# Kernel optimization log

Measured on AMD Instinct MI355X. Metric: run time of the kernel, lower is better.

The kernel has to match this reference:

```python
import jax, jax.numpy as jnp
import numpy as np

MAXHD = 100.0
MAXV = 40.0
LSTM_UNITS = 20
IN_DIM = 12


def setup_inputs() -> dict:
    key = jax.random.key(0)
    ks = jax.random.split(key, 10)
    nveh, nt = 8192, 512
    leadfol_inputs = jax.random.normal(ks[0], (nveh, nt, IN_DIM), dtype=jnp.float32)
    true_traj = jax.random.normal(ks[1], (nveh, nt), dtype=jnp.float32)
    hidden_states = jnp.zeros((2, nveh, LSTM_UNITS), dtype=jnp.float32)
    s = 0.1
    # LSTM kernel/recurrent kernel/bias (keras gate order: i, f, c, o)
    W_k = jax.random.normal(ks[2], (IN_DIM, 4 * LSTM_UNITS), dtype=jnp.float32) * s
    W_r = jax.random.normal(ks[3], (LSTM_UNITS, 4 * LSTM_UNITS), dtype=jnp.float32) * s
    b_l = jnp.zeros((4 * LSTM_UNITS,), dtype=jnp.float32)
    # dense (10, relu) and lc_actions (3)
    W_d = jax.random.normal(ks[4], (LSTM_UNITS, 10), dtype=jnp.float32) * s
    b_d = jnp.zeros((10,), dtype=jnp.float32)
    W_lc = jax.random.normal(ks[5], (10, 3), dtype=jnp.float32) * s
    b_lc = jnp.zeros((3,), dtype=jnp.float32)
    return {"leadfol_inputs": leadfol_inputs, "true_traj": true_traj,
            "hidden_states": hidden_states, "W_k": W_k, "W_r": W_r, "b_l": b_l,
            "W_d": W_d, "b_d": b_d, "W_lc": W_lc, "b_lc": b_lc}


def reference(leadfol_inputs, true_traj, hidden_states, W_k, W_r, b_l, W_d, b_d, W_lc, b_lc):
    # time-major for scan: (nt, nveh, ...)
    lf_t = jnp.swapaxes(leadfol_inputs, 0, 1)
    pos_t = jnp.swapaxes(true_traj, 0, 1)

    def step(carry, xt):
        h, c = carry
        pos, lf = xt  # pos: (nveh,), lf: (nveh, 12)
        lead_hd = (lf[:, :3] - pos[:, None]) / MAXHD
        fol_hd = (pos[:, None] - lf[:, 3:6]) / MAXHD
        spds = lf[:, 6:] / MAXV
        x = jnp.concatenate([lead_hd, fol_hd, spds], axis=1)
        x = jnp.where(jnp.isnan(x), jnp.ones_like(x), x)
        z = x @ W_k + h @ W_r + b_l
        zi, zf, zg, zo = jnp.split(z, 4, axis=1)
        c = jax.nn.sigmoid(zf) * c + jax.nn.sigmoid(zi) * jnp.tanh(zg)
        h = jax.nn.sigmoid(zo) * jnp.tanh(c)
        d = jax.nn.relu(h @ W_d + b_d)
        lc = d @ W_lc + b_lc
        return (h, c), lc

    (h, c), lc_t = jax.lax.scan(step, (hidden_states[0], hidden_states[1]), (pos_t, lf_t))
    pred_lc_action = jnp.swapaxes(lc_t, 0, 1)  # (nveh, nt, 3)
    return (true_traj, pred_lc_action, h, c)
```

## Files before the change

### kernel.cpp

```cpp
#include <hip/hip_runtime.h>

#define NVEH 8192
#define NT   512

typedef short bf16x8 __attribute__((ext_vector_type(8)));
typedef float f32x4  __attribute__((ext_vector_type(4)));

__device__ __forceinline__ float fsig(float x) {
    float e = __builtin_amdgcn_exp2f(-1.44269504f * x);
    return __builtin_amdgcn_rcpf(1.0f + e);
}
__device__ __forceinline__ float ftanh(float x) {
    float e = __builtin_amdgcn_exp2f(-2.88539008f * x);
    return 2.0f * __builtin_amdgcn_rcpf(1.0f + e) - 1.0f;
}
__device__ __forceinline__ unsigned short f2bf(float f) {
    union { float f; unsigned u; } vv; vv.f = f;
    unsigned r = vv.u + 0x7fff + ((vv.u >> 16) & 1);
    return (unsigned short)(r >> 16);
}

__device__ __forceinline__ void lds_barrier() {
    asm volatile("s_waitcnt lgkmcnt(0)" ::: "memory");
    __builtin_amdgcn_s_barrier();
    asm volatile("" ::: "memory");
}

__global__ __launch_bounds__(256) void lstm_scan_kernel(
    const float* __restrict__ lead, const float* __restrict__ traj,
    const float* __restrict__ hidden,
    const float* __restrict__ W_k, const float* __restrict__ W_r,
    const float* __restrict__ b_l, const float* __restrict__ W_d,
    const float* __restrict__ b_d, const float* __restrict__ W_lc,
    const float* __restrict__ b_lc,
    float* __restrict__ out_lc, float* __restrict__ out_h, float* __restrict__ out_c)
{
    __shared__ alignas(16) unsigned short row[2][16][40];

    const int tid  = threadIdx.x;
    const int wid  = tid >> 6;
    const int lane = tid & 63;
    const int q    = lane >> 4;
    const int v    = lane & 15;
    const int gv   = blockIdx.x * 16 + v;

    const int ntile = (wid < 2) ? 2 : (wid == 2) ? 1 : 0;

    bf16x8 aW[2]; f32x4 cB[2];
    float h32[2], cst[2];
    int uu[2];
    #pragma unroll
    for (int l = 0; l < 2; ++l) {
        if (l < ntile) {
            const int tt = 2 * wid + l;
            #pragma unroll
            for (int j = 0; j < 8; ++j) {
                int k  = q * 8 + j;
                int qv = v >> 2, rv = v & 3;
                int u  = (tt < 4) ? (8 * (tt >> 1) + 2 * qv + (tt & 1)) : (16 + qv);
                int col = rv * 20 + u;
                float w = (k < 12) ? W_k[k * 80 + col] : W_r[(k - 12) * 80 + col];
                aW[l][j] = (short)f2bf(w);
            }
            uu[l] = (tt < 4) ? (8 * (tt >> 1) + 2 * q + (tt & 1)) : (16 + q);
            #pragma unroll
            for (int reg = 0; reg < 4; ++reg)
                cB[l][reg] = b_l[reg * 20 + uu[l]];
            h32[l] = hidden[(size_t)gv * 20 + uu[l]];
            cst[l] = hidden[(size_t)NVEH * 20 + (size_t)gv * 20 + uu[l]];
        }
    }

    if (wid < 2) {
        unsigned pk = (unsigned)f2bf(h32[0]) | ((unsigned)f2bf(h32[1]) << 16);
        *(unsigned*)&row[0][v][12 + 8 * wid + 2 * q] = pk;
    } else if (wid == 2) {
        row[0][v][28 + q] = f2bf(h32[0]);
    }

    const float* lf = lead + (size_t)gv * NT * 12;
    const float* ps = traj + (size_t)gv * NT;
    float* lcout    = out_lc + (size_t)gv * NT * 3;

    bf16x8 aH = {}; f32x4 cD = {};
    float wlc[4][3] = {}; float pb0[3] = {};
    float Ac[4], Bc[4];
    float4 rA = make_float4(0.f,0.f,0.f,0.f), rB = rA, rC = rA;
    float pA = 0.f, pB = 0.f, pC = 0.f;
    if (wid == 3) {
        #pragma unroll
        for (int j = 0; j < 8; ++j) {
            int k = q * 8 + j;
            aH[j] = (v < 10 && k >= 12) ? (short)f2bf(W_d[(k - 12) * 10 + v]) : (short)0;
        }
        #pragma unroll
        for (int reg = 0; reg < 4; ++reg) {
            int m = 4 * q + reg;
            cD[reg] = (m < 10) ? b_d[m] : 0.0f;
            #pragma unroll
            for (int j = 0; j < 3; ++j)
                wlc[reg][j] = (m < 10) ? W_lc[m * 3 + j] : 0.0f;
        }
        #pragma unroll
        for (int j = 0; j < 3; ++j) pb0[j] = (q == 0) ? b_lc[j] : 0.0f;

        #pragma unroll
        for (int i = 0; i < 4; ++i) {
            int e = 4 * q + i;
            if (e < 3)      { Ac[i] =  0.01f;  Bc[i] = -0.01f; }
            else if (e < 6) { Ac[i] = -0.01f;  Bc[i] =  0.01f; }
            else            { Ac[i] =  0.025f; Bc[i] =  0.0f;  }
        }

        #pragma unroll
        for (int s = 0; s < 2; ++s) {
            float4 r0 = make_float4(0.f,0.f,0.f,0.f); float p0s = 0.f;
            if (q < 3) r0 = *(const float4*)(lf + 12 * s + q * 4);
            if (q < 2) p0s = ps[s];
            if (q < 3) {
                float xv[4] = { r0.x, r0.y, r0.z, r0.w };
                #pragma unroll
                for (int i = 0; i < 4; ++i) {
                    float x = fmaf(xv[i], Ac[i], p0s * Bc[i]);
                    xv[i] = (x == x) ? x : 1.0f;
                }
                unsigned pk0 = (unsigned)f2bf(xv[0]) | ((unsigned)f2bf(xv[1]) << 16);
                unsigned pk1 = (unsigned)f2bf(xv[2]) | ((unsigned)f2bf(xv[3]) << 16);
                *(uint2*)&row[s][v][4 * q] = make_uint2(pk0, pk1);
            }
        }
        if (q < 3) {
            rA = *(const float4*)(lf + 12 * 2 + q * 4);
            rB = *(const float4*)(lf + 12 * 3 + q * 4);
            rC = *(const float4*)(lf + 12 * 4 + q * 4);
        }
        if (q < 2) { pA = ps[2]; pB = ps[3]; pC = ps[4]; }
    }

    lds_barrier();
    bf16x8 bx = *(const bf16x8*)&row[0][v][8 * q];

    for (int t = 0; t < NT; ++t) {
        const int nxt = (t + 1) & 1;

        if (wid < 3) {
            f32x4 z0 = __builtin_amdgcn_mfma_f32_16x16x32_bf16(aW[0], bx, cB[0], 0, 0, 0);
            f32x4 z1;
            if (ntile == 2)
                z1 = __builtin_amdgcn_mfma_f32_16x16x32_bf16(aW[1], bx, cB[1], 0, 0, 0);

            {
                float si = fsig(z0[0]);
                float sf = fsig(z0[1]);
                float tg = ftanh(z0[2]);
                float so = fsig(z0[3]);
                float cn = fmaf(sf, cst[0], si * tg);
                cst[0] = cn;
                h32[0] = so * ftanh(cn);
            }
            if (ntile == 2) {
                float si = fsig(z1[0]);
                float sf = fsig(z1[1]);
                float tg = ftanh(z1[2]);
                float so = fsig(z1[3]);
                float cn = fmaf(sf, cst[1], si * tg);
                cst[1] = cn;
                h32[1] = so * ftanh(cn);
            }

            if (wid < 2) {
                unsigned pk = (unsigned)f2bf(h32[0]) | ((unsigned)f2bf(h32[1]) << 16);
                *(unsigned*)&row[nxt][v][12 + 8 * wid + 2 * q] = pk;
            } else {
                row[nxt][v][28 + q] = f2bf(h32[0]);
            }
        }

        lds_barrier();
        bf16x8 bxn = *(const bf16x8*)&row[nxt][v][8 * q];

        if (wid == 3) {
            f32x4 d = __builtin_amdgcn_mfma_f32_16x16x32_bf16(aH, bxn, cD, 0, 0, 0);
            float dr[4];
            #pragma unroll
            for (int reg = 0; reg < 4; ++reg) dr[reg] = fmaxf(d[reg], 0.0f);
            float p[3];
            #pragma unroll
            for (int j = 0; j < 3; ++j) {
                float acc = pb0[j];
                #pragma unroll
                for (int reg = 0; reg < 4; ++reg) acc = fmaf(dr[reg], wlc[reg][j], acc);
                acc += __shfl_xor(acc, 16);
                acc += __shfl_xor(acc, 32);
                p[j] = acc;
            }
            if (q == (t & 3)) {
                float* o = lcout + (size_t)t * 3;
                *(float2*)o = make_float2(p[0], p[1]);
                o[2] = p[2];
            }

            if (q < 3) {
                float xv[4] = { rA.x, rA.y, rA.z, rA.w };
                #pragma unroll
                for (int i = 0; i < 4; ++i) {
                    float x = fmaf(xv[i], Ac[i], pA * Bc[i]);
                    xv[i] = (x == x) ? x : 1.0f;
                }
                unsigned pk0 = (unsigned)f2bf(xv[0]) | ((unsigned)f2bf(xv[1]) << 16);
                unsigned pk1 = (unsigned)f2bf(xv[2]) | ((unsigned)f2bf(xv[3]) << 16);
                *(uint2*)&row[t & 1][v][4 * q] = make_uint2(pk0, pk1);
            }
            rA = rB; rB = rC; pA = pB; pB = pC;
            int tn = (t + 5 < NT) ? (t + 5) : (NT - 1);
            if (q < 3) rC = *(const float4*)(lf + 12 * tn + q * 4);
            if (q < 2) pC = ps[tn];
        }

        bx = bxn;
    }

    if (wid < 3) {
        #pragma unroll
        for (int l = 0; l < 2; ++l) {
            if (l < ntile) {
                out_h[(size_t)gv * 20 + uu[l]] = h32[l];
                out_c[(size_t)gv * 20 + uu[l]] = cst[l];
            }
        }
    }
}

extern "C" void kernel_launch(void* const* d_in, const int* in_sizes, int n_in,
                              void* d_out, int out_size, void* d_ws, size_t ws_size,
                              hipStream_t stream) {
    const float* lead   = (const float*)d_in[0];
    const float* traj   = (const float*)d_in[1];
    const float* hidden = (const float*)d_in[2];
    const float* W_k    = (const float*)d_in[3];
    const float* W_r    = (const float*)d_in[4];
    const float* b_l    = (const float*)d_in[5];
    const float* W_d    = (const float*)d_in[6];
    const float* b_d    = (const float*)d_in[7];
    const float* W_lc   = (const float*)d_in[8];
    const float* b_lc   = (const float*)d_in[9];

    float* out    = (float*)d_out;
    float* out_tt = out;
    float* out_lc = out + (size_t)NVEH * NT;
    float* out_h  = out_lc + (size_t)NVEH * NT * 3;
    float* out_c  = out_h + (size_t)NVEH * 20;

    hipMemcpyAsync(out_tt, traj, (size_t)NVEH * NT * sizeof(float),
                   hipMemcpyDeviceToDevice, stream);

    lstm_scan_kernel<<<dim3(NVEH / 16), dim3(256), 0, stream>>>(
        lead, traj, hidden, W_k, W_r, b_l, W_d, b_d, W_lc, b_lc,
        out_lc, out_h, out_c);
}
```

Before: 657.6 us.

## Process two 16-vehicle groups per block to interleave independent recurrences

Each block now handles two independent groups of 16 vehicles, issuing their MFMAs and gate math back to back so one group's latency can hide behind the other's. This amortises the per-timestep barrier over twice the work and halves the grid size. It also switches the packed h conversion to the hardware v_cvt_pk_bf16_f32 instruction. The cost is higher register use, fewer blocks (256 versus 512), and a longer serial epilogue in the output-producing wave.

```diff
diff --git a/kernel.cpp b/kernel.cpp
--- a/kernel.cpp
+++ b/kernel.cpp
@@ -2,6 +2,7 @@
 
 #define NVEH 8192
 #define NT   512
+#define G    2
 
 typedef short bf16x8 __attribute__((ext_vector_type(8)));
 typedef float f32x4  __attribute__((ext_vector_type(4)));
@@ -18,6 +19,11 @@
     union { float f; unsigned u; } vv; vv.f = f;
     unsigned r = vv.u + 0x7fff + ((vv.u >> 16) & 1);
     return (unsigned short)(r >> 16);
+}
+__device__ __forceinline__ unsigned cvtpk_bf16(float lo, float hi) {
+    unsigned r;
+    asm("v_cvt_pk_bf16_f32 %0, %1, %2" : "=v"(r) : "v"(lo), "v"(hi));
+    return r;
 }
 
 __device__ __forceinline__ void lds_barrier() {
@@ -35,19 +41,22 @@
     const float* __restrict__ b_lc,
     float* __restrict__ out_lc, float* __restrict__ out_h, float* __restrict__ out_c)
 {
-    __shared__ alignas(16) unsigned short row[2][16][40];
+    __shared__ alignas(16) unsigned short row[G][2][16][40];
 
     const int tid  = threadIdx.x;
     const int wid  = tid >> 6;
     const int lane = tid & 63;
     const int q    = lane >> 4;
     const int v    = lane & 15;
-    const int gv   = blockIdx.x * 16 + v;
+
+    int gv[G];
+    #pragma unroll
+    for (int g = 0; g < G; ++g) gv[g] = blockIdx.x * (16 * G) + g * 16 + v;
 
     const int ntile = (wid < 2) ? 2 : (wid == 2) ? 1 : 0;
 
     bf16x8 aW[2]; f32x4 cB[2];
-    float h32[2], cst[2];
+    float h32[G][2], cst[G][2];
     int uu[2];
     #pragma unroll
     for (int l = 0; l < 2; ++l) {
@@ -66,27 +75,42 @@
             #pragma unroll
             for (int reg = 0; reg < 4; ++reg)
                 cB[l][reg] = b_l[reg * 20 + uu[l]];
-            h32[l] = hidden[(size_t)gv * 20 + uu[l]];
-            cst[l] = hidden[(size_t)NVEH * 20 + (size_t)gv * 20 + uu[l]];
-        }
-    }
-
-    if (wid < 2) {
-        unsigned pk = (unsigned)f2bf(h32[0]) | ((unsigned)f2bf(h32[1]) << 16);
-        *(unsigned*)&row[0][v][12 + 8 * wid + 2 * q] = pk;
-    } else if (wid == 2) {
-        row[0][v][28 + q] = f2bf(h32[0]);
-    }
-
-    const float* lf = lead + (size_t)gv * NT * 12;
-    const float* ps = traj + (size_t)gv * NT;
-    float* lcout    = out_lc + (size_t)gv * NT * 3;
+            #pragma unroll
+            for (int g = 0; g < G; ++g) {
+                h32[g][l] = hidden[(size_t)gv[g] * 20 + uu[l]];
+                cst[g][l] = hidden[(size_t)NVEH * 20 + (size_t)gv[g] * 20 + uu[l]];
+            }
+        }
+    }
+
+    #pragma unroll
+    for (int g = 0; g < G; ++g) {
+        if (wid < 2) {
+            unsigned pk = cvtpk_bf16(h32[g][0], h32[g][1]);
+            *(unsigned*)&row[g][0][v][12 + 8 * wid + 2 * q] = pk;
+        } else if (wid == 2) {
+            row[g][0][v][28 + q] = f2bf(h32[g][0]);
+        }
+    }
+
+    const float* lf[G]; const float* ps[G]; float* lcout[G];
+    #pragma unroll
+    for (int g = 0; g < G; ++g) {
+        lf[g]    = lead + (size_t)gv[g] * NT * 12;
+        ps[g]    = traj + (size_t)gv[g] * NT;
+        lcout[g] = out_lc + (size_t)gv[g] * NT * 3;
+    }
 
     bf16x8 aH = {}; f32x4 cD = {};
     float wlc[4][3] = {}; float pb0[3] = {};
     float Ac[4], Bc[4];
-    float4 rA = make_float4(0.f,0.f,0.f,0.f), rB = rA, rC = rA;
-    float pA = 0.f, pB = 0.f, pC = 0.f;
+    float4 rA[G], rB[G], rC[G];
+    float pA[G], pB[G], pC[G];
+    #pragma unroll
+    for (int g = 0; g < G; ++g) {
+        rA[g] = make_float4(0.f,0.f,0.f,0.f); rB[g] = rA[g]; rC[g] = rA[g];
+        pA[g] = pB[g] = pC[g] = 0.f;
+    }
     if (wid == 3) {
         #pragma unroll
         for (int j = 0; j < 8; ++j) {
@@ -113,119 +137,138 @@
         }
 
         #pragma unroll
-        for (int s = 0; s < 2; ++s) {
-            float4 r0 = make_float4(0.f,0.f,0.f,0.f); float p0s = 0.f;
-            if (q < 3) r0 = *(const float4*)(lf + 12 * s + q * 4);
-            if (q < 2) p0s = ps[s];
+        for (int g = 0; g < G; ++g) {
+            #pragma unroll
+            for (int s = 0; s < 2; ++s) {
+                float4 r0 = make_float4(0.f,0.f,0.f,0.f); float p0s = 0.f;
+                if (q < 3) r0 = *(const float4*)(lf[g] + 12 * s + q * 4);
+                if (q < 2) p0s = ps[g][s];
+                if (q < 3) {
+                    float xv[4] = { r0.x, r0.y, r0.z, r0.w };
+                    #pragma unroll
+                    for (int i = 0; i < 4; ++i) {
+                        float x = fmaf(xv[i], Ac[i], p0s * Bc[i]);
+                        xv[i] = (x == x) ? x : 1.0f;
+                    }
+                    unsigned pk0 = (unsigned)f2bf(xv[0]) | ((unsigned)f2bf(xv[1]) << 16);
+                    unsigned pk1 = (unsigned)f2bf(xv[2]) | ((unsigned)f2bf(xv[3]) << 16);
+                    *(uint2*)&row[g][s][v][4 * q] = make_uint2(pk0, pk1);
+                }
+            }
             if (q < 3) {
-                float xv[4] = { r0.x, r0.y, r0.z, r0.w };
-                #pragma unroll
-                for (int i = 0; i < 4; ++i) {
-                    float x = fmaf(xv[i], Ac[i], p0s * Bc[i]);
-                    xv[i] = (x == x) ? x : 1.0f;
-                }
-                unsigned pk0 = (unsigned)f2bf(xv[0]) | ((unsigned)f2bf(xv[1]) << 16);
-                unsigned pk1 = (unsigned)f2bf(xv[2]) | ((unsigned)f2bf(xv[3]) << 16);
-                *(uint2*)&row[s][v][4 * q] = make_uint2(pk0, pk1);
-            }
-        }
-        if (q < 3) {
-            rA = *(const float4*)(lf + 12 * 2 + q * 4);
-            rB = *(const float4*)(lf + 12 * 3 + q * 4);
-            rC = *(const float4*)(lf + 12 * 4 + q * 4);
-        }
-        if (q < 2) { pA = ps[2]; pB = ps[3]; pC = ps[4]; }
+                rA[g] = *(const float4*)(lf[g] + 12 * 2 + q * 4);
+                rB[g] = *(const float4*)(lf[g] + 12 * 3 + q * 4);
+                rC[g] = *(const float4*)(lf[g] + 12 * 4 + q * 4);
+            }
+            if (q < 2) { pA[g] = ps[g][2]; pB[g] = ps[g][3]; pC[g] = ps[g][4]; }
+        }
     }
 
     lds_barrier();
-    bf16x8 bx = *(const bf16x8*)&row[0][v][8 * q];
+    bf16x8 bx[G];
+    #pragma unroll
+    for (int g = 0; g < G; ++g) bx[g] = *(const bf16x8*)&row[g][0][v][8 * q];
 
     for (int t = 0; t < NT; ++t) {
         const int nxt = (t + 1) & 1;
 
         if (wid < 3) {
-            f32x4 z0 = __builtin_amdgcn_mfma_f32_16x16x32_bf16(aW[0], bx, cB[0], 0, 0, 0);
-            f32x4 z1;
-            if (ntile == 2)
-                z1 = __builtin_amdgcn_mfma_f32_16x16x32_bf16(aW[1], bx, cB[1], 0, 0, 0);
-
-            {
-                float si = fsig(z0[0]);
-                float sf = fsig(z0[1]);
-                float tg = ftanh(z0[2]);
-                float so = fsig(z0[3]);
-                float cn = fmaf(sf, cst[0], si * tg);
-                cst[0] = cn;
-                h32[0] = so * ftanh(cn);
-            }
-            if (ntile == 2) {
-                float si = fsig(z1[0]);
-                float sf = fsig(z1[1]);
-                float tg = ftanh(z1[2]);
-                float so = fsig(z1[3]);
-                float cn = fmaf(sf, cst[1], si * tg);
-                cst[1] = cn;
-                h32[1] = so * ftanh(cn);
-            }
-
-            if (wid < 2) {
-                unsigned pk = (unsigned)f2bf(h32[0]) | ((unsigned)f2bf(h32[1]) << 16);
-                *(unsigned*)&row[nxt][v][12 + 8 * wid + 2 * q] = pk;
-            } else {
-                row[nxt][v][28 + q] = f2bf(h32[0]);
+            f32x4 z0[G], z1[G];
+            #pragma unroll
+            for (int g = 0; g < G; ++g) {
+                z0[g] = __builtin_amdgcn_mfma_f32_16x16x32_bf16(aW[0], bx[g], cB[0], 0, 0, 0);
+                if (ntile == 2)
+                    z1[g] = __builtin_amdgcn_mfma_f32_16x16x32_bf16(aW[1], bx[g], cB[1], 0, 0, 0);
+            }
+            #pragma unroll
+            for (int g = 0; g < G; ++g) {
+                {
+                    float si = fsig(z0[g][0]);
+                    float sf = fsig(z0[g][1]);
+                    float tg = ftanh(z0[g][2]);
+                    float so = fsig(z0[g][3]);
+                    float cn = fmaf(sf, cst[g][0], si * tg);
+                    cst[g][0] = cn;
+                    h32[g][0] = so * ftanh(cn);
+                }
+                if (ntile == 2) {
+                    float si = fsig(z1[g][0]);
+                    float sf = fsig(z1[g][1]);
+                    float tg = ftanh(z1[g][2]);
+                    float so = fsig(z1[g][3]);
+                    float cn = fmaf(sf, cst[g][1], si * tg);
+                    cst[g][1] = cn;
+                    h32[g][1] = so * ftanh(cn);
+                }
+                if (wid < 2) {
+                    unsigned pk = cvtpk_bf16(h32[g][0], h32[g][1]);
+                    *(unsigned*)&row[g][nxt][v][12 + 8 * wid + 2 * q] = pk;
+                } else {
+                    row[g][nxt][v][28 + q] = f2bf(h32[g][0]);
+                }
             }
         }
 
         lds_barrier();
-        bf16x8 bxn = *(const bf16x8*)&row[nxt][v][8 * q];
+        bf16x8 bxn[G];
+        #pragma unroll
+        for (int g = 0; g < G; ++g)
+            bxn[g] = *(const bf16x8*)&row[g][nxt][v][8 * q];
 
         if (wid == 3) {
-            f32x4 d = __builtin_amdgcn_mfma_f32_16x16x32_bf16(aH, bxn, cD, 0, 0, 0);
-            float dr[4];
-            #pragma unroll
-            for (int reg = 0; reg < 4; ++reg) dr[reg] = fmaxf(d[reg], 0.0f);
-            float p[3];
-            #pragma unroll
-            for (int j = 0; j < 3; ++j) {
-                float acc = pb0[j];
+            #pragma unroll
+            for (int g = 0; g < G; ++g) {
+                f32x4 d = __builtin_amdgcn_mfma_f32_16x16x32_bf16(aH, bxn[g], cD, 0, 0, 0);
+                float dr[4];
                 #pragma unroll
-                for (int reg = 0; reg < 4; ++reg) acc = fmaf(dr[reg], wlc[reg][j], acc);
-                acc += __shfl_xor(acc, 16);
-                acc += __shfl_xor(acc, 32);
-                p[j] = acc;
-            }
-            if (q == (t & 3)) {
-                float* o = lcout + (size_t)t * 3;
-                *(float2*)o = make_float2(p[0], p[1]);
-                o[2] = p[2];
-            }
-
-            if (q < 3) {
-                float xv[4] = { rA.x, rA.y, rA.z, rA.w };
+                for (int reg = 0; reg < 4; ++reg) dr[reg] = fmaxf(d[reg], 0.0f);
+                float p[3];
                 #pragma unroll
-                for (int i = 0; i < 4; ++i) {
-                    float x = fmaf(xv[i], Ac[i], pA * Bc[i]);
-                    xv[i] = (x == x) ? x : 1.0f;
-                }
-                unsigned pk0 = (unsigned)f2bf(xv[0]) | ((unsigned)f2bf(xv[1]) << 16);
-                unsigned pk1 = (unsigned)f2bf(xv[2]) | ((unsigned)f2bf(xv[3]) << 16);
-                *(uint2*)&row[t & 1][v][4 * q] = make_uint2(pk0, pk1);
-            }
-            rA = rB; rB = rC; pA = pB; pB = pC;
-            int tn = (t + 5 < NT) ? (t + 5) : (NT - 1);
-            if (q < 3) rC = *(const float4*)(lf + 12 * tn + q * 4);
-            if (q < 2) pC = ps[tn];
-        }
-
-        bx = bxn;
+                for (int j = 0; j < 3; ++j) {
+                    float acc = pb0[j];
+                    #pragma unroll
+                    for (int reg = 0; reg < 4; ++reg) acc = fmaf(dr[reg], wlc[reg][j], acc);
+                    acc += __shfl_xor(acc, 16);
+                    acc += __shfl_xor(acc, 32);
+                    p[j] = acc;
+                }
+                if (q == (t & 3)) {
+                    float* o = lcout[g] + (size_t)t * 3;
+                    *(float2*)o = make_float2(p[0], p[1]);
+                    o[2] = p[2];
+                }
+
+                if (q < 3) {
+                    float xv[4] = { rA[g].x, rA[g].y, rA[g].z, rA[g].w };
+                    #pragma unroll
+                    for (int i = 0; i < 4; ++i) {
+                        float x = fmaf(xv[i], Ac[i], pA[g] * Bc[i]);
+                        xv[i] = (x == x) ? x : 1.0f;
+                    }
+                    unsigned pk0 = (unsigned)f2bf(xv[0]) | ((unsigned)f2bf(xv[1]) << 16);
+                    unsigned pk1 = (unsigned)f2bf(xv[2]) | ((unsigned)f2bf(xv[3]) << 16);
+                    *(uint2*)&row[g][t & 1][v][4 * q] = make_uint2(pk0, pk1);
+                }
+                rA[g] = rB[g]; rB[g] = rC[g]; pA[g] = pB[g]; pB[g] = pC[g];
+                int tn = (t + 5 < NT) ? (t + 5) : (NT - 1);
+                if (q < 3) rC[g] = *(const float4*)(lf[g] + 12 * tn + q * 4);
+                if (q < 2) pC[g] = ps[g][tn];
+            }
+        }
+
+        #pragma unroll
+        for (int g = 0; g < G; ++g) bx[g] = bxn[g];
     }
 
     if (wid < 3) {
         #pragma unroll
-        for (int l = 0; l < 2; ++l) {
-            if (l < ntile) {
-                out_h[(size_t)gv * 20 + uu[l]] = h32[l];
-                out_c[(size_t)gv * 20 + uu[l]] = cst[l];
+        for (int g = 0; g < G; ++g) {
+            #pragma unroll
+            for (int l = 0; l < 2; ++l) {
+                if (l < ntile) {
+                    out_h[(size_t)gv[g] * 20 + uu[l]] = h32[g][l];
+                    out_c[(size_t)gv[g] * 20 + uu[l]] = cst[g][l];
+                }
             }
         }
     }
@@ -254,7 +297,7 @@
     hipMemcpyAsync(out_tt, traj, (size_t)NVEH * NT * sizeof(float),
                    hipMemcpyDeviceToDevice, stream);
 
-    lstm_scan_kernel<<<dim3(NVEH / 16), dim3(256), 0, stream>>>(
+    lstm_scan_kernel<<<dim3(NVEH / (16 * G)), dim3(256), 0, stream>>>(
         lead, traj, hidden, W_k, W_r, b_l, W_d, b_d, W_lc, b_lc,
         out_lc, out_h, out_c);
 }
```

Result: slower. 773.1 us (+17.6%).

## Split LSTM gate tiles across five waves and use packed bf16 convert

Applied to the files above, without the earlier changes.

Redistributes the recurrent gate work so each of five waves handles a single 16x16 MFMA tile, with a sixth wave doing input prep and the dense head. The block grows from 256 to 384 threads, which shortens each wave's serial per-step gate chain on the critical path. The cost is more waves taking part in every per-step barrier and fewer resident blocks per CU. It also replaces the manual bf16 rounding of input features with the hardware packed convert instruction.

```diff
diff --git a/kernel.cpp b/kernel.cpp
--- a/kernel.cpp
+++ b/kernel.cpp
@@ -19,6 +19,11 @@
     unsigned r = vv.u + 0x7fff + ((vv.u >> 16) & 1);
     return (unsigned short)(r >> 16);
 }
+__device__ __forceinline__ unsigned cvtpk_bf16(float lo, float hi) {
+    unsigned r;
+    asm("v_cvt_pk_bf16_f32 %0, %1, %2" : "=v"(r) : "v"(lo), "v"(hi));
+    return r;
+}
 
 __device__ __forceinline__ void lds_barrier() {
     asm volatile("s_waitcnt lgkmcnt(0)" ::: "memory");
@@ -26,7 +31,7 @@
     asm volatile("" ::: "memory");
 }
 
-__global__ __launch_bounds__(256) void lstm_scan_kernel(
+__global__ __launch_bounds__(384) void lstm_scan_kernel(
     const float* __restrict__ lead, const float* __restrict__ traj,
     const float* __restrict__ hidden,
     const float* __restrict__ W_k, const float* __restrict__ W_r,
@@ -44,38 +49,27 @@
     const int v    = lane & 15;
     const int gv   = blockIdx.x * 16 + v;
 
-    const int ntile = (wid < 2) ? 2 : (wid == 2) ? 1 : 0;
-
-    bf16x8 aW[2]; f32x4 cB[2];
-    float h32[2], cst[2];
-    int uu[2];
-    #pragma unroll
-    for (int l = 0; l < 2; ++l) {
-        if (l < ntile) {
-            const int tt = 2 * wid + l;
-            #pragma unroll
-            for (int j = 0; j < 8; ++j) {
-                int k  = q * 8 + j;
-                int qv = v >> 2, rv = v & 3;
-                int u  = (tt < 4) ? (8 * (tt >> 1) + 2 * qv + (tt & 1)) : (16 + qv);
-                int col = rv * 20 + u;
-                float w = (k < 12) ? W_k[k * 80 + col] : W_r[(k - 12) * 80 + col];
-                aW[l][j] = (short)f2bf(w);
-            }
-            uu[l] = (tt < 4) ? (8 * (tt >> 1) + 2 * q + (tt & 1)) : (16 + q);
-            #pragma unroll
-            for (int reg = 0; reg < 4; ++reg)
-                cB[l][reg] = b_l[reg * 20 + uu[l]];
-            h32[l] = hidden[(size_t)gv * 20 + uu[l]];
-            cst[l] = hidden[(size_t)NVEH * 20 + (size_t)gv * 20 + uu[l]];
-        }
-    }
-
-    if (wid < 2) {
-        unsigned pk = (unsigned)f2bf(h32[0]) | ((unsigned)f2bf(h32[1]) << 16);
-        *(unsigned*)&row[0][v][12 + 8 * wid + 2 * q] = pk;
-    } else if (wid == 2) {
-        row[0][v][28 + q] = f2bf(h32[0]);
+    bf16x8 aW = {}; f32x4 cB = {};
+    float h32 = 0.0f, cst = 0.0f;
+    int uu = 0;
+    if (wid < 5) {
+        const int tt = wid;
+        #pragma unroll
+        for (int j = 0; j < 8; ++j) {
+            int k  = q * 8 + j;
+            int qv = v >> 2, rv = v & 3;
+            int u  = 4 * tt + qv;
+            int col = rv * 20 + u;
+            float w = (k < 12) ? W_k[k * 80 + col] : W_r[(k - 12) * 80 + col];
+            aW[j] = (short)f2bf(w);
+        }
+        uu = 4 * tt + q;
+        #pragma unroll
+        for (int reg = 0; reg < 4; ++reg)
+            cB[reg] = b_l[reg * 20 + uu];
+        h32 = hidden[(size_t)gv * 20 + uu];
+        cst = hidden[(size_t)NVEH * 20 + (size_t)gv * 20 + uu];
+        row[0][v][12 + uu] = f2bf(h32);
     }
 
     const float* lf = lead + (size_t)gv * NT * 12;
@@ -87,7 +81,7 @@
     float Ac[4], Bc[4];
     float4 rA = make_float4(0.f,0.f,0.f,0.f), rB = rA, rC = rA;
     float pA = 0.f, pB = 0.f, pC = 0.f;
-    if (wid == 3) {
+    if (wid == 5) {
         #pragma unroll
         for (int j = 0; j < 8; ++j) {
             int k = q * 8 + j;
@@ -124,9 +118,8 @@
                     float x = fmaf(xv[i], Ac[i], p0s * Bc[i]);
                     xv[i] = (x == x) ? x : 1.0f;
                 }
-                unsigned pk0 = (unsigned)f2bf(xv[0]) | ((unsigned)f2bf(xv[1]) << 16);
-                unsigned pk1 = (unsigned)f2bf(xv[2]) | ((unsigned)f2bf(xv[3]) << 16);
-                *(uint2*)&row[s][v][4 * q] = make_uint2(pk0, pk1);
+                *(uint2*)&row[s][v][4 * q] =
+                    make_uint2(cvtpk_bf16(xv[0], xv[1]), cvtpk_bf16(xv[2], xv[3]));
             }
         }
         if (q < 3) {
@@ -143,43 +136,22 @@
     for (int t = 0; t < NT; ++t) {
         const int nxt = (t + 1) & 1;
 
-        if (wid < 3) {
-            f32x4 z0 = __builtin_amdgcn_mfma_f32_16x16x32_bf16(aW[0], bx, cB[0], 0, 0, 0);
-            f32x4 z1;
-            if (ntile == 2)
-                z1 = __builtin_amdgcn_mfma_f32_16x16x32_bf16(aW[1], bx, cB[1], 0, 0, 0);
-
-            {
-                float si = fsig(z0[0]);
-                float sf = fsig(z0[1]);
-                float tg = ftanh(z0[2]);
-                float so = fsig(z0[3]);
-                float cn = fmaf(sf, cst[0], si * tg);
-                cst[0] = cn;
-                h32[0] = so * ftanh(cn);
-            }
-            if (ntile == 2) {
-                float si = fsig(z1[0]);
-                float sf = fsig(z1[1]);
-                float tg = ftanh(z1[2]);
-                float so = fsig(z1[3]);
-                float cn = fmaf(sf, cst[1], si * tg);
-                cst[1] = cn;
-                h32[1] = so * ftanh(cn);
-            }
-
-            if (wid < 2) {
-                unsigned pk = (unsigned)f2bf(h32[0]) | ((unsigned)f2bf(h32[1]) << 16);
-                *(unsigned*)&row[nxt][v][12 + 8 * wid + 2 * q] = pk;
-            } else {
-                row[nxt][v][28 + q] = f2bf(h32[0]);
-            }
+        if (wid < 5) {
+            f32x4 z = __builtin_amdgcn_mfma_f32_16x16x32_bf16(aW, bx, cB, 0, 0, 0);
+            float si = fsig(z[0]);
+            float sf = fsig(z[1]);
+            float tg = ftanh(z[2]);
+            float so = fsig(z[3]);
+            float cn = fmaf(sf, cst, si * tg);
+            cst = cn;
+            h32 = so * ftanh(cn);
+            row[nxt][v][12 + uu] = f2bf(h32);
         }
 
         lds_barrier();
         bf16x8 bxn = *(const bf16x8*)&row[nxt][v][8 * q];
 
-        if (wid == 3) {
+        if (wid == 5) {
             f32x4 d = __builtin_amdgcn_mfma_f32_16x16x32_bf16(aH, bxn, cD, 0, 0, 0);
             float dr[4];
             #pragma unroll
@@ -207,9 +179,8 @@
                     float x = fmaf(xv[i], Ac[i], pA * Bc[i]);
                     xv[i] = (x == x) ? x : 1.0f;
                 }
-                unsigned pk0 = (unsigned)f2bf(xv[0]) | ((unsigned)f2bf(xv[1]) << 16);
-                unsigned pk1 = (unsigned)f2bf(xv[2]) | ((unsigned)f2bf(xv[3]) << 16);
-                *(uint2*)&row[t & 1][v][4 * q] = make_uint2(pk0, pk1);
+                *(uint2*)&row[t & 1][v][4 * q] =
+                    make_uint2(cvtpk_bf16(xv[0], xv[1]), cvtpk_bf16(xv[2], xv[3]));
             }
             rA = rB; rB = rC; pA = pB; pB = pC;
             int tn = (t + 5 < NT) ? (t + 5) : (NT - 1);
@@ -220,14 +191,9 @@
         bx = bxn;
     }
 
-    if (wid < 3) {
-        #pragma unroll
-        for (int l = 0; l < 2; ++l) {
-            if (l < ntile) {
-                out_h[(size_t)gv * 20 + uu[l]] = h32[l];
-                out_c[(size_t)gv * 20 + uu[l]] = cst[l];
-            }
-        }
+    if (wid < 5) {
+        out_h[(size_t)gv * 20 + uu] = h32;
+        out_c[(size_t)gv * 20 + uu] = cst;
     }
 }
 
@@ -254,7 +220,7 @@
     hipMemcpyAsync(out_tt, traj, (size_t)NVEH * NT * sizeof(float),
                    hipMemcpyDeviceToDevice, stream);
 
-    lstm_scan_kernel<<<dim3(NVEH / 16), dim3(256), 0, stream>>>(
+    lstm_scan_kernel<<<dim3(NVEH / 16), dim3(384), 0, stream>>>(
         lead, traj, hidden, W_k, W_r, b_l, W_d, b_d, W_lc, b_lc,
         out_lc, out_h, out_c);
 }
```

Result: no change. 657.6 us (-0.0%).
